# Kernel tuning notes

Hardware: AMD Instinct MI355X
Metric: run time of the kernel (lower is better)

## Reference

```python
import jax, jax.numpy as jnp
import numpy as np

EPS = 1e-5  # torch BatchNorm default


def setup_inputs() -> dict:
    key = jax.random.key(0)
    ks = jax.random.split(key, 8)
    B, Q, S, C = 4, 256, 128, 256
    feats = [2 * C, 256, 64, 1]  # opt['num_features']
    inp = {
        "support_features": jax.random.normal(ks[0], (B, S, C), dtype=jnp.float32),
        "query_features": jax.random.normal(ks[1], (B, Q, C), dtype=jnp.float32),
    }
    for i in range(3):
        fan_in, fan_out = feats[i], feats[i + 1]
        std = np.sqrt(2.0 / (fan_in + fan_out))  # xavier_normal on conv weight
        inp[f"W{i}"] = jax.random.normal(ks[2 + i], (fan_out, fan_in), dtype=jnp.float32) * std
        inp[f"b{i}"] = jnp.zeros((fan_out,), dtype=jnp.float32)
        inp[f"g{i}"] = jnp.ones((fan_out,), dtype=jnp.float32)   # BN weight
        inp[f"bt{i}"] = jnp.zeros((fan_out,), dtype=jnp.float32)  # BN bias
    return inp


def _bn_relu(x, g, bt):
    # x: [B, N, C]; BatchNorm1d training-mode stats over batch and length dims
    mean = jnp.mean(x, axis=(0, 1))
    var = jnp.mean(jnp.square(x - mean), axis=(0, 1))  # biased var, as torch BN
    return jax.nn.relu((x - mean) * (g * jax.lax.rsqrt(var + EPS)) + bt)


def reference(support_features, query_features,
              W0, b0, g0, bt0, W1, b1, g1, bt1, W2, b2, g2, bt2):
    B, S, C = support_features.shape
    Q = query_features.shape[1]
    # pairwise concat: [B, Q, S, 2C]
    uq = jnp.broadcast_to(query_features[:, :, None, :], (B, Q, S, C))
    us = jnp.broadcast_to(support_features[:, None, :, :], (B, Q, S, C))
    x = jnp.concatenate([uq, us], axis=3).reshape(B, Q * S, 2 * C)
    # 1x1 conv == matmul over channel dim
    x = _bn_relu(jnp.einsum('bnc,oc->bno', x, W0) + b0, g0, bt0)
    x = _bn_relu(jnp.einsum('bnc,oc->bno', x, W1) + b1, g1, bt1)
    x = _bn_relu(jnp.einsum('bnc,oc->bno', x, W2) + b2, g2, bt2)
    # back to [B, C_out, Q, S]
    return jnp.transpose(x, (0, 2, 1)).reshape(B, -1, Q, S)
```

## Files before the change

### kernel.cpp

```cpp
#include <hip/hip_runtime.h>
#include <hip/hip_bf16.h>


typedef __attribute__((ext_vector_type(4))) float f32x4;
typedef __attribute__((ext_vector_type(8))) short s16x8;

#define BN_EPS 1e-5f
#define INV_N  (1.0f/131072.0f)

__device__ __forceinline__ unsigned pk_bf16(float a, float b) {
  float2 t; t.x = a; t.y = b;
  __hip_bfloat162 h = __float22bfloat162_rn(t);
  return *reinterpret_cast<unsigned*>(&h);
}
__device__ __forceinline__ void split2(float a, float b, unsigned& uh, unsigned& ul) {
  uh = pk_bf16(a, b);
  float ha = __uint_as_float(uh << 16);
  float hb = __uint_as_float(uh & 0xFFFF0000u);
  ul = pk_bf16(a - ha, b - hb);
}

union frag_u { s16x8 v; unsigned u[4]; };

struct Args {
  const float *Sf, *Qf, *W0, *b0, *g0, *bt0, *W1, *b1, *g1, *bt1, *W2, *b2, *g2, *bt2;
  float *Aq, *As, *ws0s, *ws1f, *ws2f, *out;
  unsigned *cnt;
};

__global__ __launch_bounds__(64) void k_g0(Args a)
{
  int bi = blockIdx.x, t = threadIdx.x;
  if (bi == 384) {
    for (int i = t; i < 2048; i += 64) a.ws1f[i] = 0.0f;
    if (t < 32) a.ws2f[t] = 0.0f;
    if (t < 2)  a.cnt[t] = 0u;
    return;
  }
  int l15 = t & 15, quad = t >> 4;
  int chunk = bi >> 2, ntile = bi & 3;
  bool isQ = (chunk < 64);
  const float* X; float* Out; int m0, koff;
  if (isQ) { m0 = chunk * 16; X = a.Qf; Out = a.Aq; koff = 0; }
  else     { m0 = (chunk - 64) * 16; X = a.Sf; Out = a.As; koff = 256; }
  int n0 = ntile * 64;

  f32x4 acc[4] = {};
#pragma unroll
  for (int ko = 0; ko < 256; ko += 32) {
    const float* row = X + (m0 + l15) * 256 + ko + quad * 8;
    f32x4 v0 = *(const f32x4*)(row);
    f32x4 v1 = *(const f32x4*)(row + 4);
    frag_u ah, al;
#pragma unroll
    for (int j = 0; j < 2; j++) {
      split2(v0[2 * j], v0[2 * j + 1], ah.u[j], al.u[j]);
      split2(v1[2 * j], v1[2 * j + 1], ah.u[2 + j], al.u[2 + j]);
    }
#pragma unroll
    for (int nt = 0; nt < 4; nt++) {
      const float* wrow = a.W0 + (n0 + nt * 16 + l15) * 512 + koff + ko + quad * 8;
      f32x4 w0v = *(const f32x4*)(wrow);
      f32x4 w1v = *(const f32x4*)(wrow + 4);
      frag_u bh, bl;
      split2(w0v[0], w0v[1], bh.u[0], bl.u[0]);
      split2(w0v[2], w0v[3], bh.u[1], bl.u[1]);
      split2(w1v[0], w1v[1], bh.u[2], bl.u[2]);
      split2(w1v[2], w1v[3], bh.u[3], bl.u[3]);
      acc[nt] = __builtin_amdgcn_mfma_f32_16x16x32_bf16(ah.v, bh.v, acc[nt], 0, 0, 0);
      acc[nt] = __builtin_amdgcn_mfma_f32_16x16x32_bf16(al.v, bh.v, acc[nt], 0, 0, 0);
      acc[nt] = __builtin_amdgcn_mfma_f32_16x16x32_bf16(ah.v, bl.v, acc[nt], 0, 0, 0);
    }
  }
#pragma unroll
  for (int nt = 0; nt < 4; nt++) {
    int o = n0 + nt * 16 + l15;
    float bias = isQ ? 0.0f : a.b0[o];
    float cs = 0, cs2 = 0;
#pragma unroll
    for (int r = 0; r < 4; r++) {
      float y = acc[nt][r] + bias;
      Out[(m0 + quad * 4 + r) * 256 + o] = y;
      cs += y; cs2 += y * y;
    }
    cs  += __shfl_xor(cs, 16);  cs  += __shfl_xor(cs, 32);
    cs2 += __shfl_xor(cs2, 16); cs2 += __shfl_xor(cs2, 32);
    if (quad == 0) {
      a.ws0s[chunk * 512 + o] = cs;
      a.ws0s[chunk * 512 + 256 + o] = cs2;
    }
  }
}

__device__ __forceinline__ void bn0_finalize(const Args& a, int t, float* sh_a0c0)
{
  int o = t;
  float sumY = 0, cross = 0, SQ2 = 0, SS2 = 0;
#pragma unroll
  for (int b = 0; b < 4; b++) {
    float sq1 = 0, sq2 = 0, ss1 = 0, ss2 = 0;
#pragma unroll
    for (int c = 0; c < 16; c++) {
      sq1 += a.ws0s[(b * 16 + c) * 512 + o];
      sq2 += a.ws0s[(b * 16 + c) * 512 + 256 + o];
    }
#pragma unroll
    for (int c = 0; c < 8; c++) {
      ss1 += a.ws0s[(64 + b * 8 + c) * 512 + o];
      ss2 += a.ws0s[(64 + b * 8 + c) * 512 + 256 + o];
    }
    SQ2 += sq2; SS2 += ss2;
    sumY += 128.0f * sq1 + 256.0f * ss1;
    cross += sq1 * ss1;
  }
  float mean = sumY * INV_N;
  float var = (128.0f * SQ2 + 256.0f * SS2 + 2.0f * cross) * INV_N - mean * mean;
  float aa = a.g0[o] * rsqrtf(var + BN_EPS);
  sh_a0c0[o] = aa;
  sh_a0c0[256 + o] = a.bt0[o] - mean * aa;
}

__device__ __forceinline__ void grid_barrier(unsigned* cnt, unsigned target, int t)
{
  asm volatile("s_waitcnt vmcnt(0)" ::: "memory");
  __syncthreads();
  if (t == 0) {
    __hip_atomic_fetch_add(cnt, 1u, __ATOMIC_RELAXED, __HIP_MEMORY_SCOPE_AGENT);
    while (__hip_atomic_load(cnt, __ATOMIC_RELAXED, __HIP_MEMORY_SCOPE_AGENT) < target)
      __builtin_amdgcn_s_sleep(8);
  }
  __syncthreads();
}

__global__ __launch_bounds__(256, 2) void k_f(Args a)
{
  int bi = blockIdx.x, t = threadIdx.x;
  int w = t >> 6, l = t & 63, l15 = l & 15, quad = l >> 4;
  __shared__ ushort w1f[2048 * 8];
  __shared__ float sh_a0c0[512];
  __shared__ float red[2][4][4][16];
  __shared__ float sh_tot[128];
  __shared__ float sh_a1c1[128];
  __shared__ float rs[16], rs2[16];
  __shared__ float sh_fin[2];

#pragma unroll
  for (int i = 0; i < 8; i++) {
    int fr = i * 256 + t;
    int kk = fr >> 8, r = fr & 255, nt = r >> 6, ln = r & 63;
    const float* src = a.W1 + (nt * 16 + (ln & 15)) * 256 + kk * 32 + (ln >> 4) * 8;
    f32x4 v0 = *(const f32x4*)(src);
    f32x4 v1 = *(const f32x4*)(src + 4);
    frag_u z;
    z.u[0] = pk_bf16(v0[0], v0[1]); z.u[1] = pk_bf16(v0[2], v0[3]);
    z.u[2] = pk_bf16(v1[0], v1[1]); z.u[3] = pk_bf16(v1[2], v1[3]);
    *(s16x8*)(w1f + fr * 8) = z.v;
  }
  bn0_finalize(a, t, sh_a0c0);
  __syncthreads();

  int b_ = bi >> 7, rem = bi & 127, qt = rem >> 3, st = rem & 7;
  const float* asrow = a.As + ((b_ << 7) + st * 16 + l15) * 256;
  const float* aqrow[4];
#pragma unroll
  for (int mt = 0; mt < 4; mt++)
    aqrow[mt] = a.Aq + ((b_ << 8) + qt * 16 + w * 4 + mt) * 256;

  f32x4 acc[4][4] = {};
#pragma unroll
  for (int kk = 0; kk < 8; kk++) {
    int obase = kk * 32 + quad * 8;
    f32x4 a0v0 = *(const f32x4*)(sh_a0c0 + obase);
    f32x4 a0v1 = *(const f32x4*)(sh_a0c0 + obase + 4);
    f32x4 c0v0 = *(const f32x4*)(sh_a0c0 + 256 + obase);
    f32x4 c0v1 = *(const f32x4*)(sh_a0c0 + 256 + obase + 4);
    f32x4 as0 = *(const f32x4*)(asrow + obase);
    f32x4 as1 = *(const f32x4*)(asrow + obase + 4);

    s16x8 zh[4];
#pragma unroll
    for (int mt = 0; mt < 4; mt++) {
      f32x4 aq0 = *(const f32x4*)(aqrow[mt] + obase);
      f32x4 aq1 = *(const f32x4*)(aqrow[mt] + obase + 4);
      f32x4 z0 = (aq0 + as0) * a0v0 + c0v0;
      f32x4 z1 = (aq1 + as1) * a0v1 + c0v1;
      frag_u zz;
      zz.u[0] = pk_bf16(fmaxf(z0[0], 0.0f), fmaxf(z0[1], 0.0f));
      zz.u[1] = pk_bf16(fmaxf(z0[2], 0.0f), fmaxf(z0[3], 0.0f));
      zz.u[2] = pk_bf16(fmaxf(z1[0], 0.0f), fmaxf(z1[1], 0.0f));
      zz.u[3] = pk_bf16(fmaxf(z1[2], 0.0f), fmaxf(z1[3], 0.0f));
      zh[mt] = zz.v;
    }
#pragma unroll
    for (int nt = 0; nt < 4; nt++) {
      s16x8 bw = *(const s16x8*)(w1f + ((kk * 4 + nt) * 64 + l) * 8);
#pragma unroll
      for (int mt = 0; mt < 4; mt++)
        acc[mt][nt] = __builtin_amdgcn_mfma_f32_16x16x32_bf16(zh[mt], bw, acc[mt][nt], 0, 0, 0);
    }
  }

  float biasv[4];
#pragma unroll
  for (int nt = 0; nt < 4; nt++) biasv[nt] = a.b1[nt * 16 + l15];
  unsigned ku01[4][4], ku23[4][4];
  float s[4] = {0, 0, 0, 0}, s2[4] = {0, 0, 0, 0};
#pragma unroll
  for (int mt = 0; mt < 4; mt++) {
#pragma unroll
    for (int nt = 0; nt < 4; nt++) {
      float y0 = acc[mt][nt][0] + biasv[nt];
      float y1 = acc[mt][nt][1] + biasv[nt];
      float y2v = acc[mt][nt][2] + biasv[nt];
      float y3 = acc[mt][nt][3] + biasv[nt];
      unsigned u01 = pk_bf16(y0, y1), u23 = pk_bf16(y2v, y3);
      ku01[mt][nt] = u01; ku23[mt][nt] = u23;
      float f0 = __uint_as_float(u01 << 16), f1 = __uint_as_float(u01 & 0xFFFF0000u);
      float f2 = __uint_as_float(u23 << 16), f3 = __uint_as_float(u23 & 0xFFFF0000u);
      s[nt]  += f0 + f1 + f2 + f3;
      s2[nt] += f0 * f0 + f1 * f1 + f2 * f2 + f3 * f3;
    }
  }
#pragma unroll
  for (int nt = 0; nt < 4; nt++) {
    float v = s[nt], v2 = s2[nt];
    v  += __shfl_xor(v, 16);  v  += __shfl_xor(v, 32);
    v2 += __shfl_xor(v2, 16); v2 += __shfl_xor(v2, 32);
    if (quad == 0) { red[0][w][nt][l15] = v; red[1][w][nt][l15] = v2; }
  }
  __syncthreads();
  if (t < 128) {
    int which = t >> 6, j = t & 63, nt = j >> 4, jl = j & 15;
    float v = red[which][0][nt][jl] + red[which][1][nt][jl] +
              red[which][2][nt][jl] + red[which][3][nt][jl];
    atomicAdd(&a.ws1f[(bi & 15) * 128 + t], v);
  }

  grid_barrier(&a.cnt[0], 512u, t);

  if (t < 128) {
    float accv = 0;
#pragma unroll
    for (int c = 0; c < 16; c++)
      accv += __hip_atomic_load(&a.ws1f[c * 128 + t], __ATOMIC_RELAXED, __HIP_MEMORY_SCOPE_AGENT);
    sh_tot[t] = accv;
  }
  __syncthreads();
  if (t < 64) {
    float mean = sh_tot[t] * INV_N;
    float var = sh_tot[64 + t] * INV_N - mean * mean;
    float aa = a.g1[t] * rsqrtf(var + BN_EPS);
    sh_a1c1[t] = aa;
    sh_a1c1[64 + t] = a.bt1[t] - mean * aa;
  }
  __syncthreads();

  float a1v[4], c1v[4], w2v[4];
#pragma unroll
  for (int nt = 0; nt < 4; nt++) {
    int j = nt * 16 + l15;
    a1v[nt] = sh_a1c1[j]; c1v[nt] = sh_a1c1[64 + j]; w2v[nt] = a.W2[j];
  }
  float b2v = a.b2[0];
  float y2k[4][4];
  float ls = 0, ls2 = 0;
#pragma unroll
  for (int mt = 0; mt < 4; mt++) {
    float part[4] = {0, 0, 0, 0};
#pragma unroll
    for (int nt = 0; nt < 4; nt++) {
      unsigned u01 = ku01[mt][nt], u23 = ku23[mt][nt];
      float f0 = __uint_as_float(u01 << 16), f1 = __uint_as_float(u01 & 0xFFFF0000u);
      float f2 = __uint_as_float(u23 << 16), f3 = __uint_as_float(u23 & 0xFFFF0000u);
      part[0] += fmaxf(a1v[nt] * f0 + c1v[nt], 0.0f) * w2v[nt];
      part[1] += fmaxf(a1v[nt] * f1 + c1v[nt], 0.0f) * w2v[nt];
      part[2] += fmaxf(a1v[nt] * f2 + c1v[nt], 0.0f) * w2v[nt];
      part[3] += fmaxf(a1v[nt] * f3 + c1v[nt], 0.0f) * w2v[nt];
    }
#pragma unroll
    for (int r = 0; r < 4; r++) {
      float pv = part[r];
      pv += __shfl_xor(pv, 1); pv += __shfl_xor(pv, 2);
      pv += __shfl_xor(pv, 4); pv += __shfl_xor(pv, 8);
      float y = pv + b2v;
      y2k[mt][r] = y;
      if (l15 == 0) { ls += y; ls2 += y * y; }
    }
  }
  if (l15 == 0) { rs[t >> 4] = ls; rs2[t >> 4] = ls2; }
  __syncthreads();
  if (t == 0) {
    float sv = 0, sv2 = 0;
#pragma unroll
    for (int i = 0; i < 16; i++) { sv += rs[i]; sv2 += rs2[i]; }
    atomicAdd(&a.ws2f[(bi & 15) * 2], sv);
    atomicAdd(&a.ws2f[(bi & 15) * 2 + 1], sv2);
  }

  grid_barrier(&a.cnt[1], 512u, t);

  if (t == 0) {
    float sv = 0, sv2 = 0;
#pragma unroll
    for (int c = 0; c < 16; c++) {
      sv  += __hip_atomic_load(&a.ws2f[c * 2],     __ATOMIC_RELAXED, __HIP_MEMORY_SCOPE_AGENT);
      sv2 += __hip_atomic_load(&a.ws2f[c * 2 + 1], __ATOMIC_RELAXED, __HIP_MEMORY_SCOPE_AGENT);
    }
    float mean = sv * INV_N;
    float var = sv2 * INV_N - mean * mean;
    float aa = a.g2[0] * rsqrtf(var + BN_EPS);
    sh_fin[0] = aa;
    sh_fin[1] = a.bt2[0] - mean * aa;
  }
  __syncthreads();
  float aav = sh_fin[0], ccv = sh_fin[1];

#pragma unroll
  for (int mt = 0; mt < 4; mt++) {
    if (l15 == 0) {
      int q = qt * 16 + w * 4 + mt;
      int P = ((b_ * 256 + q) * 128) + st * 16 + quad * 4;
      f32x4 o;
#pragma unroll
      for (int r = 0; r < 4; r++) o[r] = fmaxf(aav * y2k[mt][r] + ccv, 0.0f);
      *(f32x4*)(a.out + P) = o;
    }
  }
}

extern "C" void kernel_launch(void* const* d_in, const int* in_sizes, int n_in,
                              void* d_out, int out_size, void* d_ws, size_t ws_size,
                              hipStream_t stream)
{
  float* ws = (float*)d_ws;
  Args a;
  a.Sf  = (const float*)d_in[0];
  a.Qf  = (const float*)d_in[1];
  a.W0  = (const float*)d_in[2];
  a.b0  = (const float*)d_in[3];
  a.g0  = (const float*)d_in[4];
  a.bt0 = (const float*)d_in[5];
  a.W1  = (const float*)d_in[6];
  a.b1  = (const float*)d_in[7];
  a.g1  = (const float*)d_in[8];
  a.bt1 = (const float*)d_in[9];
  a.W2  = (const float*)d_in[10];
  a.b2  = (const float*)d_in[11];
  a.g2  = (const float*)d_in[12];
  a.bt2 = (const float*)d_in[13];

  a.Aq   = ws;
  a.As   = ws + 262144;
  a.ws0s = ws + 524288;
  a.ws1f = ws + 573440;
  a.ws2f = ws + 575488;
  a.cnt  = (unsigned*)(ws + 575520);
  a.out  = (float*)d_out;

  k_g0<<<385, 64, 0, stream>>>(a);
  k_f <<<512, 256, 0, stream>>>(a);
}
```

Measured before the change: 142.4 us.

## Replace flat grid barriers with hierarchical counters and last-block finalize broadcast

Replaces the two single-counter grid barriers with a two-level arrival tree: 16 leaf counters, each reached by 32 blocks, feed a root counter. The last block to arrive finalizes the BN1 and BN2 statistics and publishes the results through replicated slots and per-group gate flags. The other blocks spin on their own gate and read the precomputed scale and shift instead of each re-reducing the partial sums. The BN1 partial-sum buffer is widened from 16 to 32 slots to reduce atomic contention. The cost is an extra serial finalize step on a single block between arrival and release.

After: 126.9 us. 1.12x faster.

```diff
diff --git a/kernel.cpp b/kernel.cpp
--- a/kernel.cpp
+++ b/kernel.cpp
@@ -7,6 +7,15 @@
 
 #define BN_EPS 1e-5f
 #define INV_N  (1.0f/131072.0f)
+
+#define LEAFA(g)   ((g)*16)
+#define ROOTA      256
+#define GATEA(g)   (272 + (g)*16)
+#define REP_A      1024
+#define LEAFB(g)   (5120 + (g)*16)
+#define ROOTB      5376
+#define GATEB(g)   (5392 + (g)*16)
+#define CNT_ZERO   5696
 
 __device__ __forceinline__ unsigned pk_bf16(float a, float b) {
   float2 t; t.x = a; t.y = b;
@@ -20,6 +29,19 @@
   ul = pk_bf16(a - ha, b - hb);
 }
 
+__device__ __forceinline__ unsigned a_ld(const unsigned* p) {
+  return __hip_atomic_load(p, __ATOMIC_RELAXED, __HIP_MEMORY_SCOPE_AGENT);
+}
+__device__ __forceinline__ float a_ldf(const float* p) {
+  return __hip_atomic_load(p, __ATOMIC_RELAXED, __HIP_MEMORY_SCOPE_AGENT);
+}
+__device__ __forceinline__ void a_st(unsigned* p, unsigned v) {
+  __hip_atomic_store(p, v, __ATOMIC_RELAXED, __HIP_MEMORY_SCOPE_AGENT);
+}
+__device__ __forceinline__ unsigned a_add(unsigned* p) {
+  return __hip_atomic_fetch_add(p, 1u, __ATOMIC_RELAXED, __HIP_MEMORY_SCOPE_AGENT);
+}
+
 union frag_u { s16x8 v; unsigned u[4]; };
 
 struct Args {
@@ -32,9 +54,9 @@
 {
   int bi = blockIdx.x, t = threadIdx.x;
   if (bi == 384) {
-    for (int i = t; i < 2048; i += 64) a.ws1f[i] = 0.0f;
+    for (int i = t; i < 4096; i += 64) a.ws1f[i] = 0.0f;
     if (t < 32) a.ws2f[t] = 0.0f;
-    if (t < 2)  a.cnt[t] = 0u;
+    for (int i = t; i < CNT_ZERO; i += 64) a.cnt[i] = 0u;
     return;
   }
   int l15 = t & 15, quad = t >> 4;
@@ -120,18 +142,6 @@
   sh_a0c0[256 + o] = a.bt0[o] - mean * aa;
 }
 
-__device__ __forceinline__ void grid_barrier(unsigned* cnt, unsigned target, int t)
-{
-  asm volatile("s_waitcnt vmcnt(0)" ::: "memory");
-  __syncthreads();
-  if (t == 0) {
-    __hip_atomic_fetch_add(cnt, 1u, __ATOMIC_RELAXED, __HIP_MEMORY_SCOPE_AGENT);
-    while (__hip_atomic_load(cnt, __ATOMIC_RELAXED, __HIP_MEMORY_SCOPE_AGENT) < target)
-      __builtin_amdgcn_s_sleep(8);
-  }
-  __syncthreads();
-}
-
 __global__ __launch_bounds__(256, 2) void k_f(Args a)
 {
   int bi = blockIdx.x, t = threadIdx.x;
@@ -143,6 +153,7 @@
   __shared__ float sh_a1c1[128];
   __shared__ float rs[16], rs2[16];
   __shared__ float sh_fin[2];
+  __shared__ int s_finA;
 
 #pragma unroll
   for (int i = 0; i < 8; i++) {
@@ -233,26 +244,59 @@
     int which = t >> 6, j = t & 63, nt = j >> 4, jl = j & 15;
     float v = red[which][0][nt][jl] + red[which][1][nt][jl] +
               red[which][2][nt][jl] + red[which][3][nt][jl];
-    atomicAdd(&a.ws1f[(bi & 15) * 128 + t], v);
-  }
-
-  grid_barrier(&a.cnt[0], 512u, t);
-
-  if (t < 128) {
-    float accv = 0;
-#pragma unroll
-    for (int c = 0; c < 16; c++)
-      accv += __hip_atomic_load(&a.ws1f[c * 128 + t], __ATOMIC_RELAXED, __HIP_MEMORY_SCOPE_AGENT);
-    sh_tot[t] = accv;
-  }
-  __syncthreads();
-  if (t < 64) {
-    float mean = sh_tot[t] * INV_N;
-    float var = sh_tot[64 + t] * INV_N - mean * mean;
-    float aa = a.g1[t] * rsqrtf(var + BN_EPS);
-    sh_a1c1[t] = aa;
-    sh_a1c1[64 + t] = a.bt1[t] - mean * aa;
-  }
+    atomicAdd(&a.ws1f[(bi & 31) * 128 + t], v);
+  }
+
+  asm volatile("s_waitcnt vmcnt(0)" ::: "memory");
+  __syncthreads();
+  if (t == 0) {
+    int g = bi & 15;
+    unsigned old = a_add(&a.cnt[LEAFA(g)]);
+    int fin = 0;
+    if (old == 31u) {
+      unsigned r = a_add(&a.cnt[ROOTA]);
+      fin = (r == 15u);
+    }
+    s_finA = fin;
+  }
+  __syncthreads();
+  if (s_finA) {
+    if (t < 128) {
+      float accv = 0;
+#pragma unroll
+      for (int c = 0; c < 32; c++)
+        accv += a_ldf(&a.ws1f[c * 128 + t]);
+      sh_tot[t] = accv;
+    }
+    __syncthreads();
+    if (t < 64) {
+      float mean = sh_tot[t] * INV_N;
+      float var = sh_tot[64 + t] * INV_N - mean * mean;
+      float aa = a.g1[t] * rsqrtf(var + BN_EPS);
+      sh_a1c1[t] = aa;
+      sh_a1c1[64 + t] = a.bt1[t] - mean * aa;
+    }
+    __syncthreads();
+    if (t < 128) {
+      unsigned uv = __float_as_uint(sh_a1c1[t]);
+#pragma unroll
+      for (int r = 0; r < 32; r++)
+        a_st(&a.cnt[REP_A + r * 128 + t], uv);
+    }
+    asm volatile("s_waitcnt vmcnt(0)" ::: "memory");
+    __syncthreads();
+    if (t == 0) {
+#pragma unroll
+      for (int i = 0; i < 16; i++) a_st(&a.cnt[GATEA(i)], 1u);
+    }
+  }
+  if (t == 0) {
+    int g = bi & 15;
+    while (a_ld(&a.cnt[GATEA(g)]) == 0u) __builtin_amdgcn_s_sleep(32);
+  }
+  __syncthreads();
+  if (t < 128)
+    sh_a1c1[t] = __uint_as_float(a_ld(&a.cnt[REP_A + (bi & 31) * 128 + t]));
   __syncthreads();
 
   float a1v[4], c1v[4], w2v[4];
@@ -297,20 +341,39 @@
     atomicAdd(&a.ws2f[(bi & 15) * 2 + 1], sv2);
   }
 
-  grid_barrier(&a.cnt[1], 512u, t);
-
+  asm volatile("s_waitcnt vmcnt(0)" ::: "memory");
+  __syncthreads();
   if (t == 0) {
-    float sv = 0, sv2 = 0;
-#pragma unroll
-    for (int c = 0; c < 16; c++) {
-      sv  += __hip_atomic_load(&a.ws2f[c * 2],     __ATOMIC_RELAXED, __HIP_MEMORY_SCOPE_AGENT);
-      sv2 += __hip_atomic_load(&a.ws2f[c * 2 + 1], __ATOMIC_RELAXED, __HIP_MEMORY_SCOPE_AGENT);
-    }
-    float mean = sv * INV_N;
-    float var = sv2 * INV_N - mean * mean;
-    float aa = a.g2[0] * rsqrtf(var + BN_EPS);
-    sh_fin[0] = aa;
-    sh_fin[1] = a.bt2[0] - mean * aa;
+    int g = bi & 15;
+    unsigned old = a_add(&a.cnt[LEAFB(g)]);
+    if (old == 31u) {
+      unsigned r = a_add(&a.cnt[ROOTB]);
+      if (r == 15u) {
+        float sv = 0, sv2 = 0;
+#pragma unroll
+        for (int c = 0; c < 16; c++) {
+          sv  += a_ldf(&a.ws2f[c * 2]);
+          sv2 += a_ldf(&a.ws2f[c * 2 + 1]);
+        }
+        float mean = sv * INV_N;
+        float var = sv2 * INV_N - mean * mean;
+        float aa = a.g2[0] * rsqrtf(var + BN_EPS);
+        float cc = a.bt2[0] - mean * aa;
+        unsigned ua = __float_as_uint(aa), uc = __float_as_uint(cc);
+#pragma unroll
+        for (int i = 0; i < 16; i++) {
+          a_st(&a.cnt[GATEB(i) + 1], ua);
+          a_st(&a.cnt[GATEB(i) + 2], uc);
+        }
+        asm volatile("s_waitcnt vmcnt(0)" ::: "memory");
+#pragma unroll
+        for (int i = 0; i < 16; i++) a_st(&a.cnt[GATEB(i)], 1u);
+      }
+    }
+    int gg = bi & 15;
+    while (a_ld(&a.cnt[GATEB(gg)]) == 0u) __builtin_amdgcn_s_sleep(32);
+    sh_fin[0] = __uint_as_float(a_ld(&a.cnt[GATEB(gg) + 1]));
+    sh_fin[1] = __uint_as_float(a_ld(&a.cnt[GATEB(gg) + 2]));
   }
   __syncthreads();
   float aav = sh_fin[0], ccv = sh_fin[1];
@@ -353,8 +416,8 @@
   a.As   = ws + 262144;
   a.ws0s = ws + 524288;
   a.ws1f = ws + 573440;
-  a.ws2f = ws + 575488;
-  a.cnt  = (unsigned*)(ws + 575520);
+  a.ws2f = ws + 577536;
+  a.cnt  = (unsigned*)(ws + 577568);
   a.out  = (float*)d_out;
 
   k_g0<<<385, 64, 0, stream>>>(a);
```
